# Performance work log

Measured on AMD Instinct MI355X. Metric: run time of the kernel, lower is better.

## Reference

```python
import jax, jax.numpy as jnp
import numpy as np

N_HEADS = 16
EMB_DIM = 2048
HEAD_DIM = EMB_DIM // N_HEADS  # 128
SEQ_LEN = 2048


def _init_tensor(key, size, scale_dim=0):
    # matches torch: (2*rand - 1) / sqrt(size[scale_dim])
    u = jax.random.uniform(key, size, dtype=jnp.float32)
    return (2.0 * u - 1.0) / jnp.sqrt(jnp.float32(size[scale_dim]))


def setup_inputs() -> dict:
    key = jax.random.key(0)
    kx, kq, kk, kv, ko = jax.random.split(key, 5)
    X = jax.random.normal(kx, (1, SEQ_LEN, EMB_DIM), dtype=jnp.float32)
    W_Q = _init_tensor(kq, (N_HEADS, EMB_DIM, HEAD_DIM), scale_dim=1)
    W_K = _init_tensor(kk, (N_HEADS, EMB_DIM, HEAD_DIM), scale_dim=1)
    W_V = _init_tensor(kv, (N_HEADS, EMB_DIM, HEAD_DIM), scale_dim=1)
    W_out = _init_tensor(ko, (EMB_DIM, EMB_DIM), scale_dim=0)
    return {"X": X, "W_Q": W_Q, "W_K": W_K, "W_V": W_V, "W_out": W_out}


def reference(X, W_Q, W_K, W_V, W_out):
    # X: (1, t, d); W_Q/K/V: (n, d, h); broadcast matmul -> (n, t, h)
    x = X[0]  # (t, d)
    Q = jnp.einsum('td,ndh->nth', x, W_Q)
    K = jnp.einsum('td,ndh->nth', x, W_K)
    V = jnp.einsum('td,ndh->nth', x, W_V)
    scale = 1.0 / jnp.sqrt(jnp.float32(HEAD_DIM))
    Z = jnp.einsum('nth,nsh->nts', Q, K) * scale  # (n, t, t)
    A = jax.nn.softmax(Z, axis=-1)
    R = jnp.einsum('nts,nsh->nth', A, V)  # (n, t, h)
    t = R.shape[1]
    X_cat = jnp.transpose(R, (1, 0, 2)).reshape(t, N_HEADS * HEAD_DIM)  # (t, d)
    return X_cat @ W_out  # (t, d)
```

## Files before the change

kernel.cpp:

```cpp
#include <hip/hip_runtime.h>


typedef unsigned short u16;
typedef __bf16 bf16x8 __attribute__((ext_vector_type(8)));
typedef float f32x4 __attribute__((ext_vector_type(4)));
typedef __attribute__((address_space(1))) void gvoid;
typedef __attribute__((address_space(3))) void svoid;

union B8 { uint4 u; uint2 d[2]; bf16x8 b; };

__device__ __forceinline__ u16 f2b(float f) {
  unsigned int u = __float_as_uint(f);
  unsigned int r = (u + 0x7FFFu + ((u >> 16) & 1u)) >> 16;
  return (u16)r;
}

__global__ __launch_bounds__(256) void cvt_x_kernel(const float* __restrict__ x,
                                                    u16* __restrict__ xb) {
  int i = (blockIdx.x * 256 + threadIdx.x) * 4;
  float4 v = *(const float4*)(x + i);
  ushort4 o;
  o.x = f2b(v.x); o.y = f2b(v.y); o.z = f2b(v.z); o.w = f2b(v.w);
  *(ushort4*)(xb + i) = o;
}

__global__ __launch_bounds__(256) void tcvt_kernel(const float* __restrict__ src,
                                                   u16* __restrict__ dst, int K, int N) {
  __shared__ float t[32][33];
  int bz = blockIdx.z;
  int n0 = blockIdx.x * 32, k0 = blockIdx.y * 32;
  const float* S = src + (size_t)bz * K * N;
  u16* D = dst + (size_t)bz * K * N;
  int tx = threadIdx.x, ty = threadIdx.y;
#pragma unroll
  for (int d = 0; d < 4; ++d)
    t[ty + d * 8][tx] = S[(size_t)(k0 + ty + d * 8) * N + n0 + tx];
  __syncthreads();
#pragma unroll
  for (int d = 0; d < 4; ++d)
    D[(size_t)(n0 + ty + d * 8) * K + k0 + tx] = f2b(t[tx][ty + d * 8]);
}

__device__ __forceinline__ void gemm_mainloop(const u16* Ag, const u16* Bg,
                                              u16* As, u16* Bs,
                                              f32x4 acc[4][4], int tid) {
  const int lane = tid & 63;
  const int wr = tid >> 7, wc = (tid >> 6) & 1;
  for (int k0 = 0; k0 < 2048; k0 += 64) {
    __syncthreads();
#pragma unroll
    for (int it = 0; it < 4; ++it) {
      int s = it * 256 + tid;
      int pb = s * 16;
      int lb = pb ^ ((((pb) >> 7) & 7) << 4);
      int row = lb >> 7;
      int k8 = (lb >> 4) & 7;
      const u16* ga = Ag + (size_t)row * 2048 + k0 + k8 * 8;
      const u16* gb = Bg + (size_t)row * 2048 + k0 + k8 * 8;
      char* la = (char*)As + it * 4096 + (tid & 192) * 16;
      char* lb2 = (char*)Bs + it * 4096 + (tid & 192) * 16;
      __builtin_amdgcn_global_load_lds((gvoid*)(void*)ga, (svoid*)la, 16, 0, 0);
      __builtin_amdgcn_global_load_lds((gvoid*)(void*)gb, (svoid*)lb2, 16, 0, 0);
    }
    __syncthreads();
#pragma unroll
    for (int ks = 0; ks < 2; ++ks) {
      B8 a[4], b[4];
#pragma unroll
      for (int i = 0; i < 4; ++i) {
        int rowa = wr * 64 + i * 16 + (lane & 15);
        int ba = rowa * 128 + ks * 64 + (lane >> 4) * 16;
        ba ^= (rowa & 7) << 4;
        a[i].u = *(const uint4*)((const char*)As + ba);
        int rowb = wc * 64 + i * 16 + (lane & 15);
        int bb = rowb * 128 + ks * 64 + (lane >> 4) * 16;
        bb ^= (rowb & 7) << 4;
        b[i].u = *(const uint4*)((const char*)Bs + bb);
      }
      __builtin_amdgcn_s_setprio(1);
#pragma unroll
      for (int i = 0; i < 4; ++i)
#pragma unroll
        for (int j = 0; j < 4; ++j)
          acc[i][j] = __builtin_amdgcn_mfma_f32_16x16x32_bf16(a[i].b, b[j].b, acc[i][j], 0, 0, 0);
      __builtin_amdgcn_s_setprio(0);
    }
  }
}

__global__ __launch_bounds__(256) void qkv_gemm_kernel(const u16* __restrict__ Xb,
                                                       const u16* __restrict__ Wb,
                                                       u16* __restrict__ Qb,
                                                       u16* __restrict__ Kb,
                                                       u16* __restrict__ VTb) {
  __shared__ __align__(16) u16 As[128 * 64];
  __shared__ __align__(16) u16 Bs[128 * 64];
  int tid = threadIdx.x;
  int o = blockIdx.x;
  int swz = (o & 7) * 96 + (o >> 3);
  int m0 = (swz & 15) * 128;
  int c0 = swz >> 4;
  int tau = c0 >> 4, head = c0 & 15;
  f32x4 z = {0.f, 0.f, 0.f, 0.f};
  f32x4 acc[4][4];
#pragma unroll
  for (int i = 0; i < 4; ++i)
#pragma unroll
    for (int j = 0; j < 4; ++j) acc[i][j] = z;
  gemm_mainloop(Xb + (size_t)m0 * 2048, Wb + (size_t)c0 * 128 * 2048, As, Bs, acc, tid);

  int lane = tid & 63, wr = tid >> 7, wc = (tid >> 6) & 1;
  if (tau < 2) {
    u16* Oh = ((tau == 0) ? Qb : Kb) + (size_t)head * 2048 * 128;
    float sc = (tau == 0) ? 0.08838834764831845f : 1.0f;
#pragma unroll
    for (int i = 0; i < 4; ++i) {
      int rb = m0 + wr * 64 + i * 16 + (lane >> 4) * 4;
#pragma unroll
      for (int j = 0; j < 4; ++j) {
        int col = wc * 64 + j * 16 + (lane & 15);
#pragma unroll
        for (int r = 0; r < 4; ++r)
          Oh[(size_t)(rb + r) * 128 + col] = f2b(acc[i][j][r] * sc);
      }
    }
  } else {
    u16* Vh = VTb + (size_t)head * 128 * 2048;
#pragma unroll
    for (int i = 0; i < 4; ++i) {
      int rb = m0 + wr * 64 + i * 16 + (lane >> 4) * 4;
#pragma unroll
      for (int j = 0; j < 4; ++j) {
        int col = wc * 64 + j * 16 + (lane & 15);
        ushort4 v;
        v.x = f2b(acc[i][j][0]); v.y = f2b(acc[i][j][1]);
        v.z = f2b(acc[i][j][2]); v.w = f2b(acc[i][j][3]);
        *(ushort4*)(Vh + (size_t)col * 2048 + rb) = v;
      }
    }
  }
}

__global__ __launch_bounds__(256, 2) void attn_kernel(const u16* __restrict__ Qb,
                                                      const u16* __restrict__ Kb,
                                                      const u16* __restrict__ VTb,
                                                      u16* __restrict__ Rb) {
  __shared__ __align__(16) u16 Ks[2][64 * 128];
  __shared__ __align__(16) u16 Vs[2][128 * 64];
  __shared__ __align__(16) u16 Ps[4 * 16 * 68];
  int tid = threadIdx.x, lane = tid & 63, w = tid >> 6;
  int bid = blockIdx.x;
  int swz = (bid & 7) * 64 + (bid >> 3);
  int head = swz >> 5;
  int q0 = (swz & 31) * 64;
  const u16* Qh = Qb + (size_t)head * 2048 * 128;
  const u16* Kh = Kb + (size_t)head * 2048 * 128;
  const u16* Vh = VTb + (size_t)head * 128 * 2048;

  B8 q[4];
  {
    int qrow = q0 + w * 16 + (lane & 15);
#pragma unroll
    for (int ks = 0; ks < 4; ++ks)
      q[ks].u = *(const uint4*)(Qh + (size_t)qrow * 128 + ks * 32 + (lane >> 4) * 8);
  }

  f32x4 o[8];
  f32x4 z4 = {0.f, 0.f, 0.f, 0.f};
#pragma unroll
  for (int f = 0; f < 8; ++f) o[f] = z4;
  float m_run[4] = {-1e30f, -1e30f, -1e30f, -1e30f};
  float l_run[4] = {0.f, 0.f, 0.f, 0.f};

  auto STAGE = [&](int bi, int s0) {
#pragma unroll
    for (int it2 = 0; it2 < 4; ++it2) {
      int pb = (it2 * 256 + tid) * 16;
      int lbK = pb ^ (((pb >> 8) & 7) << 4);
      int rowK = lbK >> 8;
      int k8 = (lbK >> 4) & 15;
      const u16* gk = Kh + (size_t)(s0 + rowK) * 128 + k8 * 8;
      char* dk = (char*)Ks[bi] + it2 * 4096 + (tid & 192) * 16;
      __builtin_amdgcn_global_load_lds((gvoid*)(void*)gk, (svoid*)dk, 16, 0, 0);
      int lbV = pb ^ (((pb >> 7) & 7) << 4);
      int rowV = lbV >> 7;
      int t8 = (lbV >> 4) & 7;
      const u16* gv = Vh + (size_t)rowV * 2048 + s0 + t8 * 8;
      char* dv = (char*)Vs[bi] + it2 * 4096 + (tid & 192) * 16;
      __builtin_amdgcn_global_load_lds((gvoid*)(void*)gv, (svoid*)dv, 16, 0, 0);
    }
  };

  STAGE(0, 0);
  __syncthreads();

  u16* Pw = Ps + w * 16 * 68;
  for (int it = 0; it < 32; ++it) {
    int cur = it & 1;
    if (it < 31) STAGE(cur ^ 1, (it + 1) * 64);

    f32x4 s[4];
#pragma unroll
    for (int f = 0; f < 4; ++f) s[f] = z4;
    __builtin_amdgcn_s_setprio(1);
#pragma unroll
    for (int f = 0; f < 4; ++f) {
      int r = f * 16 + (lane & 15);
#pragma unroll
      for (int ks = 0; ks < 4; ++ks) {
        int lb = r * 256 + ks * 64 + (lane >> 4) * 16;
        B8 kb;
        kb.u = *(const uint4*)((const char*)Ks[cur] + (lb ^ ((r & 7) << 4)));
        s[f] = __builtin_amdgcn_mfma_f32_16x16x32_bf16(q[ks].b, kb.b, s[f], 0, 0, 0);
      }
    }
    __builtin_amdgcn_s_setprio(0);

    float mt[4];
#pragma unroll
    for (int i = 0; i < 4; ++i)
      mt[i] = fmaxf(fmaxf(s[0][i], s[1][i]), fmaxf(s[2][i], s[3][i]));
#pragma unroll
    for (int mask = 1; mask <= 8; mask <<= 1)
#pragma unroll
      for (int i = 0; i < 4; ++i) mt[i] = fmaxf(mt[i], __shfl_xor(mt[i], mask, 64));

    float al[4];
#pragma unroll
    for (int i = 0; i < 4; ++i) {
      float mn = fmaxf(m_run[i], mt[i]);
      al[i] = __expf(m_run[i] - mn);
      m_run[i] = mn;
    }
    float ps[4] = {0.f, 0.f, 0.f, 0.f};
#pragma unroll
    for (int f = 0; f < 4; ++f)
#pragma unroll
      for (int i = 0; i < 4; ++i) {
        float p = __expf(s[f][i] - m_run[i]);
        ps[i] += p;
        Pw[((lane >> 4) * 4 + i) * 68 + f * 16 + (lane & 15)] = f2b(p);
      }
#pragma unroll
    for (int mask = 1; mask <= 8; mask <<= 1)
#pragma unroll
      for (int i = 0; i < 4; ++i) ps[i] += __shfl_xor(ps[i], mask, 64);
#pragma unroll
    for (int i = 0; i < 4; ++i) l_run[i] = l_run[i] * al[i] + ps[i];

#pragma unroll
    for (int f = 0; f < 8; ++f)
#pragma unroll
      for (int i = 0; i < 4; ++i) o[f][i] *= al[i];

    B8 pa[2];
#pragma unroll
    for (int k2 = 0; k2 < 2; ++k2) {
      const u16* pp = Pw + (lane & 15) * 68 + k2 * 32 + (lane >> 4) * 8;
      pa[k2].d[0] = *(const uint2*)(pp);
      pa[k2].d[1] = *(const uint2*)(pp + 4);
    }
    __builtin_amdgcn_s_setprio(1);
#pragma unroll
    for (int f = 0; f < 8; ++f) {
      int r = f * 16 + (lane & 15);
#pragma unroll
      for (int k2 = 0; k2 < 2; ++k2) {
        int lb = r * 128 + k2 * 64 + (lane >> 4) * 16;
        B8 vb;
        vb.u = *(const uint4*)((const char*)Vs[cur] + (lb ^ ((r & 7) << 4)));
        o[f] = __builtin_amdgcn_mfma_f32_16x16x32_bf16(pa[k2].b, vb.b, o[f], 0, 0, 0);
      }
    }
    __builtin_amdgcn_s_setprio(0);

    __syncthreads();
  }

#pragma unroll
  for (int i = 0; i < 4; ++i) {
    float inv = 1.0f / l_run[i];
    int row = q0 + w * 16 + (lane >> 4) * 4 + i;
#pragma unroll
    for (int f = 0; f < 8; ++f) {
      int col = head * 128 + f * 16 + (lane & 15);
      Rb[(size_t)row * 2048 + col] = f2b(o[f][i] * inv);
    }
  }
}

__global__ __launch_bounds__(256) void out_gemm_kernel(const u16* __restrict__ Rb,
                                                       const u16* __restrict__ Wob,
                                                       float* __restrict__ out) {
  __shared__ __align__(16) u16 As[128 * 64];
  __shared__ __align__(16) u16 Bs[128 * 64];
  int tid = threadIdx.x;
  int o = blockIdx.x;
  int swz = (o & 7) * 32 + (o >> 3);
  int m0 = (swz & 15) * 128, n0 = (swz >> 4) * 128;
  f32x4 z = {0.f, 0.f, 0.f, 0.f};
  f32x4 acc[4][4];
#pragma unroll
  for (int i = 0; i < 4; ++i)
#pragma unroll
    for (int j = 0; j < 4; ++j) acc[i][j] = z;
  gemm_mainloop(Rb + (size_t)m0 * 2048, Wob + (size_t)n0 * 2048, As, Bs, acc, tid);

  int lane = tid & 63, wr = tid >> 7, wc = (tid >> 6) & 1;
#pragma unroll
  for (int i = 0; i < 4; ++i) {
    int rb = m0 + wr * 64 + i * 16 + (lane >> 4) * 4;
#pragma unroll
    for (int j = 0; j < 4; ++j) {
      int col = n0 + wc * 64 + j * 16 + (lane & 15);
#pragma unroll
      for (int r = 0; r < 4; ++r)
        out[(size_t)(rb + r) * 2048 + col] = acc[i][j][r];
    }
  }
}

extern "C" void kernel_launch(void* const* d_in, const int* in_sizes, int n_in,
                              void* d_out, int out_size, void* d_ws, size_t ws_size,
                              hipStream_t stream) {
  const float* X  = (const float*)d_in[0];
  const float* WQ = (const float*)d_in[1];
  const float* WK = (const float*)d_in[2];
  const float* WV = (const float*)d_in[3];
  const float* WO = (const float*)d_in[4];
  float* out = (float*)d_out;

  char* ws = (char*)d_ws;
  const size_t MB8 = 8u << 20;
  u16* Xb    = (u16*)(ws);
  u16* Wqkvb = (u16*)(ws + MB8);
  u16* Woutb = (u16*)(ws + 4 * MB8);
  u16* Qb    = (u16*)(ws + 5 * MB8);
  u16* Kb    = (u16*)(ws + 6 * MB8);
  u16* VTb   = (u16*)(ws + 7 * MB8);
  u16* Rbuf  = (u16*)(ws + MB8);

  cvt_x_kernel<<<dim3(4096), dim3(256), 0, stream>>>(X, Xb);
  tcvt_kernel<<<dim3(4, 64, 16), dim3(32, 8), 0, stream>>>(WQ, Wqkvb, 2048, 128);
  tcvt_kernel<<<dim3(4, 64, 16), dim3(32, 8), 0, stream>>>(WK, Wqkvb + (size_t)16 * 128 * 2048, 2048, 128);
  tcvt_kernel<<<dim3(4, 64, 16), dim3(32, 8), 0, stream>>>(WV, Wqkvb + (size_t)32 * 128 * 2048, 2048, 128);
  tcvt_kernel<<<dim3(64, 64, 1), dim3(32, 8), 0, stream>>>(WO, Woutb, 2048, 2048);

  qkv_gemm_kernel<<<dim3(768), dim3(256), 0, stream>>>(Xb, Wqkvb, Qb, Kb, VTb);
  attn_kernel<<<dim3(512), dim3(256), 0, stream>>>(Qb, Kb, VTb, Rbuf);
  out_gemm_kernel<<<dim3(256), dim3(256), 0, stream>>>(Rbuf, Woutb, out);
}
```

Measured before the change: 326.8 us.

## Merge conversion kernels into one launch and double-buffer output GEMM LDS

Replaces the five separate conversion and transpose launches (X cast plus four weight transposes) with a single prep kernel that picks its segment from the block index. This removes launch overhead and the gaps between small kernels. Separately, the output projection GEMM now uses a double-buffered LDS mainloop, so the next K-tile is prefetched while the current one is computed, with one barrier per iteration instead of two. The price is twice the LDS per block in out_gemm, which may lower occupancy.

Measured after the change: 315.9 us. 1.03x faster.

```diff
diff --git a/kernel.cpp b/kernel.cpp
--- a/kernel.cpp
+++ b/kernel.cpp
@@ -15,30 +15,97 @@
   return (u16)r;
 }
 
-__global__ __launch_bounds__(256) void cvt_x_kernel(const float* __restrict__ x,
-                                                    u16* __restrict__ xb) {
-  int i = (blockIdx.x * 256 + threadIdx.x) * 4;
-  float4 v = *(const float4*)(x + i);
-  ushort4 o;
-  o.x = f2b(v.x); o.y = f2b(v.y); o.z = f2b(v.z); o.w = f2b(v.w);
-  *(ushort4*)(xb + i) = o;
-}
-
-__global__ __launch_bounds__(256) void tcvt_kernel(const float* __restrict__ src,
-                                                   u16* __restrict__ dst, int K, int N) {
+__global__ __launch_bounds__(256) void prep_kernel(const float* __restrict__ X,
+                                                   const float* __restrict__ WQ,
+                                                   const float* __restrict__ WK,
+                                                   const float* __restrict__ WV,
+                                                   const float* __restrict__ WO,
+                                                   u16* __restrict__ Xb,
+                                                   u16* __restrict__ Wqkvb,
+                                                   u16* __restrict__ Woutb) {
+  int bid = blockIdx.x;
+  int seg = bid >> 12;
+  int sub = bid & 4095;
+  int tid = threadIdx.x;
+  if (seg == 0) {
+    int i = (sub * 256 + tid) * 4;
+    float4 v = *(const float4*)(X + i);
+    ushort4 o;
+    o.x = f2b(v.x); o.y = f2b(v.y); o.z = f2b(v.z); o.w = f2b(v.w);
+    *(ushort4*)(Xb + i) = o;
+    return;
+  }
   __shared__ float t[32][33];
-  int bz = blockIdx.z;
-  int n0 = blockIdx.x * 32, k0 = blockIdx.y * 32;
-  const float* S = src + (size_t)bz * K * N;
-  u16* D = dst + (size_t)bz * K * N;
-  int tx = threadIdx.x, ty = threadIdx.y;
+  const float* S;
+  u16* D;
+  int N, n0, k0;
+  if (seg <= 3) {
+    const float* W = (seg == 1) ? WQ : (seg == 2) ? WK : WV;
+    int head = sub >> 8, rest = sub & 255;
+    N = 128;
+    S = W + (size_t)head * 2048 * 128;
+    D = Wqkvb + (size_t)(seg - 1) * 16 * 2048 * 128 + (size_t)head * 2048 * 128;
+    n0 = (rest & 3) * 32;
+    k0 = (rest >> 2) * 32;
+  } else {
+    N = 2048;
+    S = WO;
+    D = Woutb;
+    n0 = (sub & 63) * 32;
+    k0 = (sub >> 6) * 32;
+  }
+  int tx = tid & 31, ty = tid >> 5;
 #pragma unroll
   for (int d = 0; d < 4; ++d)
     t[ty + d * 8][tx] = S[(size_t)(k0 + ty + d * 8) * N + n0 + tx];
   __syncthreads();
 #pragma unroll
   for (int d = 0; d < 4; ++d)
-    D[(size_t)(n0 + ty + d * 8) * K + k0 + tx] = f2b(t[tx][ty + d * 8]);
+    D[(size_t)(n0 + ty + d * 8) * 2048 + k0 + tx] = f2b(t[tx][ty + d * 8]);
+}
+
+__device__ __forceinline__ void stage_tile(const u16* Ag, const u16* Bg,
+                                           u16* As, u16* Bs, int k0, int tid) {
+#pragma unroll
+  for (int it = 0; it < 4; ++it) {
+    int s = it * 256 + tid;
+    int pb = s * 16;
+    int lb = pb ^ ((((pb) >> 7) & 7) << 4);
+    int row = lb >> 7;
+    int k8 = (lb >> 4) & 7;
+    const u16* ga = Ag + (size_t)row * 2048 + k0 + k8 * 8;
+    const u16* gb = Bg + (size_t)row * 2048 + k0 + k8 * 8;
+    char* la = (char*)As + it * 4096 + (tid & 192) * 16;
+    char* lb2 = (char*)Bs + it * 4096 + (tid & 192) * 16;
+    __builtin_amdgcn_global_load_lds((gvoid*)(void*)ga, (svoid*)la, 16, 0, 0);
+    __builtin_amdgcn_global_load_lds((gvoid*)(void*)gb, (svoid*)lb2, 16, 0, 0);
+  }
+}
+
+__device__ __forceinline__ void compute_tile(const u16* As, const u16* Bs,
+                                             f32x4 acc[4][4], int lane, int wr, int wc) {
+#pragma unroll
+  for (int ks = 0; ks < 2; ++ks) {
+    B8 a[4], b[4];
+#pragma unroll
+    for (int i = 0; i < 4; ++i) {
+      int rowa = wr * 64 + i * 16 + (lane & 15);
+      int ba = rowa * 128 + ks * 64 + (lane >> 4) * 16;
+      ba ^= (rowa & 7) << 4;
+      a[i].u = *(const uint4*)((const char*)As + ba);
+      int rowb = wc * 64 + i * 16 + (lane & 15);
+      int bb = rowb * 128 + ks * 64 + (lane >> 4) * 16;
+      bb ^= (rowb & 7) << 4;
+      b[i].u = *(const uint4*)((const char*)Bs + bb);
+    }
+    __builtin_amdgcn_s_setprio(1);
+#pragma unroll
+    for (int i = 0; i < 4; ++i)
+#pragma unroll
+      for (int j = 0; j < 4; ++j)
+        acc[i][j] = __builtin_amdgcn_mfma_f32_16x16x32_bf16(a[i].b, b[j].b, acc[i][j], 0, 0, 0);
+    __builtin_amdgcn_s_setprio(0);
+  }
 }
 
 __device__ __forceinline__ void gemm_mainloop(const u16* Ag, const u16* Bg,
@@ -48,43 +115,27 @@
   const int wr = tid >> 7, wc = (tid >> 6) & 1;
   for (int k0 = 0; k0 < 2048; k0 += 64) {
     __syncthreads();
-#pragma unroll
-    for (int it = 0; it < 4; ++it) {
-      int s = it * 256 + tid;
-      int pb = s * 16;
-      int lb = pb ^ ((((pb) >> 7) & 7) << 4);
-      int row = lb >> 7;
-      int k8 = (lb >> 4) & 7;
-      const u16* ga = Ag + (size_t)row * 2048 + k0 + k8 * 8;
-      const u16* gb = Bg + (size_t)row * 2048 + k0 + k8 * 8;
-      char* la = (char*)As + it * 4096 + (tid & 192) * 16;
-      char* lb2 = (char*)Bs + it * 4096 + (tid & 192) * 16;
-      __builtin_amdgcn_global_load_lds((gvoid*)(void*)ga, (svoid*)la, 16, 0, 0);
-      __builtin_amdgcn_global_load_lds((gvoid*)(void*)gb, (svoid*)lb2, 16, 0, 0);
-    }
+    stage_tile(Ag, Bg, As, Bs, k0, tid);
     __syncthreads();
-#pragma unroll
-    for (int ks = 0; ks < 2; ++ks) {
-      B8 a[4], b[4];
-#pragma unroll
-      for (int i = 0; i < 4; ++i) {
-        int rowa = wr * 64 + i * 16 + (lane & 15);
-        int ba = rowa * 128 + ks * 64 + (lane >> 4) * 16;
-        ba ^= (rowa & 7) << 4;
-        a[i].u = *(const uint4*)((const char*)As + ba);
-        int rowb = wc * 64 + i * 16 + (lane & 15);
-        int bb = rowb * 128 + ks * 64 + (lane >> 4) * 16;
-        bb ^= (rowb & 7) << 4;
-        b[i].u = *(const uint4*)((const char*)Bs + bb);
-      }
-      __builtin_amdgcn_s_setprio(1);
-#pragma unroll
-      for (int i = 0; i < 4; ++i)
-#pragma unroll
-        for (int j = 0; j < 4; ++j)
-          acc[i][j] = __builtin_amdgcn_mfma_f32_16x16x32_bf16(a[i].b, b[j].b, acc[i][j], 0, 0, 0);
-      __builtin_amdgcn_s_setprio(0);
-    }
+    compute_tile(As, Bs, acc, lane, wr, wc);
+  }
+}
+
+__device__ __forceinline__ void gemm_mainloop_dbuf(const u16* Ag, const u16* Bg,
+                                                   u16* As0, u16* Bs0, u16* As1, u16* Bs1,
+                                                   f32x4 acc[4][4], int tid) {
+  const int lane = tid & 63;
+  const int wr = tid >> 7, wc = (tid >> 6) & 1;
+  stage_tile(Ag, Bg, As0, Bs0, 0, tid);
+  __syncthreads();
+  for (int i = 0; i < 32; ++i) {
+    u16* Ac = (i & 1) ? As1 : As0;
+    u16* Bc = (i & 1) ? Bs1 : Bs0;
+    u16* An = (i & 1) ? As0 : As1;
+    u16* Bn = (i & 1) ? Bs0 : Bs1;
+    if (i < 31) stage_tile(Ag, Bg, An, Bn, (i + 1) * 64, tid);
+    compute_tile(Ac, Bc, acc, lane, wr, wc);
+    __syncthreads();
   }
 }
 
@@ -292,8 +343,8 @@
 __global__ __launch_bounds__(256) void out_gemm_kernel(const u16* __restrict__ Rb,
                                                        const u16* __restrict__ Wob,
                                                        float* __restrict__ out) {
-  __shared__ __align__(16) u16 As[128 * 64];
-  __shared__ __align__(16) u16 Bs[128 * 64];
+  __shared__ __align__(16) u16 As[2][128 * 64];
+  __shared__ __align__(16) u16 Bs[2][128 * 64];
   int tid = threadIdx.x;
   int o = blockIdx.x;
   int swz = (o & 7) * 32 + (o >> 3);
@@ -304,7 +355,8 @@
   for (int i = 0; i < 4; ++i)
 #pragma unroll
     for (int j = 0; j < 4; ++j) acc[i][j] = z;
-  gemm_mainloop(Rb + (size_t)m0 * 2048, Wob + (size_t)n0 * 2048, As, Bs, acc, tid);
+  gemm_mainloop_dbuf(Rb + (size_t)m0 * 2048, Wob + (size_t)n0 * 2048,
+                     As[0], Bs[0], As[1], Bs[1], acc, tid);
 
   int lane = tid & 63, wr = tid >> 7, wc = (tid >> 6) & 1;
 #pragma unroll
@@ -340,12 +392,7 @@
   u16* VTb   = (u16*)(ws + 7 * MB8);
   u16* Rbuf  = (u16*)(ws + MB8);
 
-  cvt_x_kernel<<<dim3(4096), dim3(256), 0, stream>>>(X, Xb);
-  tcvt_kernel<<<dim3(4, 64, 16), dim3(32, 8), 0, stream>>>(WQ, Wqkvb, 2048, 128);
-  tcvt_kernel<<<dim3(4, 64, 16), dim3(32, 8), 0, stream>>>(WK, Wqkvb + (size_t)16 * 128 * 2048, 2048, 128);
-  tcvt_kernel<<<dim3(4, 64, 16), dim3(32, 8), 0, stream>>>(WV, Wqkvb + (size_t)32 * 128 * 2048, 2048, 128);
-  tcvt_kernel<<<dim3(64, 64, 1), dim3(32, 8), 0, stream>>>(WO, Woutb, 2048, 2048);
-
+  prep_kernel<<<dim3(20480), dim3(256), 0, stream>>>(X, WQ, WK, WV, WO, Xb, Wqkvb, Woutb);
   qkv_gemm_kernel<<<dim3(768), dim3(256), 0, stream>>>(Xb, Wqkvb, Qb, Kb, VTb);
   attn_kernel<<<dim3(512), dim3(256), 0, stream>>>(Qb, Kb, VTb, Rbuf);
   out_gemm_kernel<<<dim3(256), dim3(256), 0, stream>>>(Rbuf, Woutb, out);
```
